# Kernel optimization log

Hardware: AMD Instinct MI355X
Metric: run time of the kernel (lower is better)

The kernel has to match this reference:

```python
import jax, jax.numpy as jnp
import numpy as np

T, B, D = 8192, 8, 512
PRIOR_COUNT = 2
EPS = 1e-5


def setup_inputs() -> dict:
    key = jax.random.key(0)
    ks = jax.random.split(key, 5)
    x = jax.random.normal(ks[0], (T, B, D), dtype=jnp.float32)
    padding_mask = jnp.zeros((B, T), dtype=bool)  # True = padded position
    prior_mean = jax.random.normal(ks[1], (D,), dtype=jnp.float32) * 0.1
    prior_logv = jax.random.normal(ks[2], (D,), dtype=jnp.float32) * 0.1
    weight = jax.random.normal(ks[3], (D,), dtype=jnp.float32) * 0.1
    bias = jax.random.normal(ks[4], (D,), dtype=jnp.float32) * 0.1
    return {"x": x, "prior_mean": prior_mean, "prior_logv": prior_logv,
            "weight": weight, "bias": bias, "padding_mask": padding_mask}


def reference(x, prior_mean, prior_logv, weight, bias, padding_mask):
    # x: (T, B, D); padding_mask: (B, T) with True = pad.
    # Per-timestep Welford running mean/variance (carried across time, skipping
    # padded steps) followed by affine normalization: the TimestepNorm forward.
    gamma = weight + 1.0
    beta = bias
    b = x.shape[1]
    count0 = jnp.full((b,), PRIOR_COUNT, dtype=x.dtype)
    mean0 = jnp.broadcast_to(prior_mean, (b, D)).astype(x.dtype)
    var0 = jnp.broadcast_to(jnp.exp(prior_logv), (b, D)).astype(x.dtype)
    mask_tb = padding_mask.T  # (T, B)

    def step(carry, inp):
        count, mean, var = carry
        xt, mt = inp                                  # xt: (B, D), mt: (B,)
        valid = (~mt).astype(xt.dtype)                # 1 if real token, 0 if pad
        c_new = count + valid
        coef = valid / c_new                          # 0 on padded steps
        delta = xt - mean
        mean_new = mean + coef[:, None] * delta
        # Welford variance update: var += (delta*(x - mean_new) - var)/count
        var_new = var + coef[:, None] * (delta * (xt - mean_new) - var)
        y = (xt - mean_new) * jax.lax.rsqrt(var_new + EPS) * gamma + beta
        return (c_new, mean_new, var_new), y

    (_, _, _), ys = jax.lax.scan(step, (count0, mean0, var0), (x, mask_tb))
    return ys  # (T, B, D), same layout as module output
```

## Files before the change

kernel.cpp:

```cpp
#include <hip/hip_runtime.h>
#include <math.h>


#define T_DIM 8192
#define B_DIM 8
#define D_DIM 512
#define NC    128
#define CT    (T_DIM / NC)
#define BD    (B_DIM * D_DIM)
#define C0    2.0f
#define EPS   1e-5f


__global__ __launch_bounds__(128) void ts_pass1(
    const float* __restrict__ x, const unsigned char* __restrict__ mask,
    float* __restrict__ s1p, float* __restrict__ s2p, float* __restrict__ cnt) {
  const int chunk = blockIdx.x;
  const int b     = blockIdx.y;
  const int tid   = threadIdx.x;
  const int t0    = chunk * CT;
  const float4* xp = (const float4*)x;
  const unsigned char* mrow = mask + b * T_DIM + t0;

  float s1x = 0.f, s1y = 0.f, s1z = 0.f, s1w = 0.f;
  float s2x = 0.f, s2y = 0.f, s2z = 0.f, s2w = 0.f;
  float c = 0.f;
#pragma unroll 4
  for (int i = 0; i < CT; ++i) {
    float valid = mrow[i] ? 0.f : 1.f;
    float4 v = xp[((t0 + i) * B_DIM + b) * (D_DIM / 4) + tid];
    c += valid;
    s1x += valid * v.x; s2x += valid * v.x * v.x;
    s1y += valid * v.y; s2y += valid * v.y * v.y;
    s1z += valid * v.z; s2z += valid * v.z * v.z;
    s1w += valid * v.w; s2w += valid * v.w * v.w;
  }
  const int pidx = chunk * (BD / 4) + b * (D_DIM / 4) + tid;
  ((float4*)s1p)[pidx] = make_float4(s1x, s1y, s1z, s1w);
  ((float4*)s2p)[pidx] = make_float4(s2x, s2y, s2z, s2w);
  if (tid == 0) cnt[chunk * B_DIM + b] = c;
}

__global__ __launch_bounds__(256) void ts_pass2(
    float* __restrict__ s1p, float* __restrict__ s2p, float* __restrict__ cnt) {
  const int gid = blockIdx.x * 256 + threadIdx.x;
  float r1 = 0.f, r2 = 0.f;
#pragma unroll 4
  for (int k = 0; k < NC; ++k) {
    const int idx = k * BD + gid;
    float a1 = s1p[idx], a2 = s2p[idx];
    s1p[idx] = r1; s2p[idx] = r2;
    r1 += a1; r2 += a2;
  }
  if (gid < B_DIM) {
    float rc = 0.f;
    for (int k = 0; k < NC; ++k) {
      float a = cnt[k * B_DIM + gid];
      cnt[k * B_DIM + gid] = rc;
      rc += a;
    }
  }
}

__global__ __launch_bounds__(128) void ts_pass3(
    const float* __restrict__ x, const unsigned char* __restrict__ mask,
    const float* __restrict__ pm, const float* __restrict__ plv,
    const float* __restrict__ w, const float* __restrict__ bias,
    const float* __restrict__ s1p, const float* __restrict__ s2p,
    const float* __restrict__ cnt, float* __restrict__ out) {
  const int chunk = blockIdx.x;
  const int b     = blockIdx.y;
  const int tid   = threadIdx.x;
  const int t0    = chunk * CT;

  float4 pm4 = ((const float4*)pm)[tid];
  float4 lv4 = ((const float4*)plv)[tid];
  float4 g4  = ((const float4*)w)[tid];
  float4 be4 = ((const float4*)bias)[tid];
  g4.x += 1.f; g4.y += 1.f; g4.z += 1.f; g4.w += 1.f;
  float M0x = C0 * pm4.x, M0y = C0 * pm4.y, M0z = C0 * pm4.z, M0w = C0 * pm4.w;
  float V2x = C0 * (__expf(lv4.x) + pm4.x * pm4.x);
  float V2y = C0 * (__expf(lv4.y) + pm4.y * pm4.y);
  float V2z = C0 * (__expf(lv4.z) + pm4.z * pm4.z);
  float V2w = C0 * (__expf(lv4.w) + pm4.w * pm4.w);

  const int pidx = chunk * (BD / 4) + b * (D_DIM / 4) + tid;
  float4 S1 = ((const float4*)s1p)[pidx];
  float4 S2 = ((const float4*)s2p)[pidx];
  float c = C0 + cnt[chunk * B_DIM + b];

  const float4* xp = (const float4*)x;
  float4* op = (float4*)out;
  const unsigned char* mrow = mask + b * T_DIM + t0;

#pragma unroll 4
  for (int i = 0; i < CT; ++i) {
    float valid = mrow[i] ? 0.f : 1.f;
    const int xi = ((t0 + i) * B_DIM + b) * (D_DIM / 4) + tid;
    float4 v = xp[xi];
    c += valid;
    float rc = __builtin_amdgcn_rcpf(c);
    float4 y;
    {
      S1.x += valid * v.x; S2.x += valid * v.x * v.x;
      float M = M0x + S1.x;
      float mean = M * rc;
      float var = (V2x + S2.x - M * M * rc) * rc;
      y.x = (v.x - mean) * __builtin_amdgcn_rsqf(var + EPS) * g4.x + be4.x;
    }
    {
      S1.y += valid * v.y; S2.y += valid * v.y * v.y;
      float M = M0y + S1.y;
      float mean = M * rc;
      float var = (V2y + S2.y - M * M * rc) * rc;
      y.y = (v.y - mean) * __builtin_amdgcn_rsqf(var + EPS) * g4.y + be4.y;
    }
    {
      S1.z += valid * v.z; S2.z += valid * v.z * v.z;
      float M = M0z + S1.z;
      float mean = M * rc;
      float var = (V2z + S2.z - M * M * rc) * rc;
      y.z = (v.z - mean) * __builtin_amdgcn_rsqf(var + EPS) * g4.z + be4.z;
    }
    {
      S1.w += valid * v.w; S2.w += valid * v.w * v.w;
      float M = M0w + S1.w;
      float mean = M * rc;
      float var = (V2w + S2.w - M * M * rc) * rc;
      y.w = (v.w - mean) * __builtin_amdgcn_rsqf(var + EPS) * g4.w + be4.w;
    }
    op[xi] = y;
  }
}

extern "C" void kernel_launch(void* const* d_in, const int* in_sizes, int n_in,
                              void* d_out, int out_size, void* d_ws, size_t ws_size,
                              hipStream_t stream) {
  const float* x    = (const float*)d_in[0];
  const float* pm   = (const float*)d_in[1];
  const float* plv  = (const float*)d_in[2];
  const float* w    = (const float*)d_in[3];
  const float* bias = (const float*)d_in[4];
  const unsigned char* mask = (const unsigned char*)d_in[5];
  float* out = (float*)d_out;

  float* s1p = (float*)d_ws;
  float* s2p = s1p + (size_t)NC * BD;
  float* cnt = s2p + (size_t)NC * BD;

  dim3 grid(NC, B_DIM);
  ts_pass1<<<grid, 128, 0, stream>>>(x, mask, s1p, s2p, cnt);
  ts_pass2<<<BD / 256, 256, 0, stream>>>(s1p, s2p, cnt);
  ts_pass3<<<grid, 128, 0, stream>>>(x, mask, pm, plv, w, bias, s1p, s2p, cnt, out);
}
```

Measured before the change: 299.5 us.

## Fold prefix scan into pass3 and preload mask bytes as 64-bit words

Removes the separate prefix-scan kernel. Each pass3 block now sums the partial sums of all earlier chunks itself before running its output loop. Both the pass1 and pass3 kernels also load the chunk's mask bytes up front as 64-bit words instead of reading a byte per step. This drops one kernel launch and its serial per-column scan over 128 chunks, but later chunks do redundant reads proportional to their chunk index, which adds roughly quadratic partial-sum traffic (mostly cache-resident).

Result: faster. 291.2 us (-2.8%).

```diff
diff --git a/kernel.cpp b/kernel.cpp
--- a/kernel.cpp
+++ b/kernel.cpp
@@ -20,14 +20,19 @@
   const int tid   = threadIdx.x;
   const int t0    = chunk * CT;
   const float4* xp = (const float4*)x;
-  const unsigned char* mrow = mask + b * T_DIM + t0;
+
+  unsigned long long mw[CT / 8];
+  const unsigned long long* m8 =
+      (const unsigned long long*)(mask + b * T_DIM + t0);
+#pragma unroll
+  for (int j = 0; j < CT / 8; ++j) mw[j] = m8[j];
 
   float s1x = 0.f, s1y = 0.f, s1z = 0.f, s1w = 0.f;
   float s2x = 0.f, s2y = 0.f, s2z = 0.f, s2w = 0.f;
   float c = 0.f;
-#pragma unroll 4
+#pragma unroll 8
   for (int i = 0; i < CT; ++i) {
-    float valid = mrow[i] ? 0.f : 1.f;
+    float valid = ((mw[i >> 3] >> ((i & 7) * 8)) & 0xffULL) ? 0.f : 1.f;
     float4 v = xp[((t0 + i) * B_DIM + b) * (D_DIM / 4) + tid];
     c += valid;
     s1x += valid * v.x; s2x += valid * v.x * v.x;
@@ -41,27 +46,6 @@
   if (tid == 0) cnt[chunk * B_DIM + b] = c;
 }
 
-__global__ __launch_bounds__(256) void ts_pass2(
-    float* __restrict__ s1p, float* __restrict__ s2p, float* __restrict__ cnt) {
-  const int gid = blockIdx.x * 256 + threadIdx.x;
-  float r1 = 0.f, r2 = 0.f;
-#pragma unroll 4
-  for (int k = 0; k < NC; ++k) {
-    const int idx = k * BD + gid;
-    float a1 = s1p[idx], a2 = s2p[idx];
-    s1p[idx] = r1; s2p[idx] = r2;
-    r1 += a1; r2 += a2;
-  }
-  if (gid < B_DIM) {
-    float rc = 0.f;
-    for (int k = 0; k < NC; ++k) {
-      float a = cnt[k * B_DIM + gid];
-      cnt[k * B_DIM + gid] = rc;
-      rc += a;
-    }
-  }
-}
-
 __global__ __launch_bounds__(128) void ts_pass3(
     const float* __restrict__ x, const unsigned char* __restrict__ mask,
     const float* __restrict__ pm, const float* __restrict__ plv,
@@ -72,6 +56,24 @@
   const int b     = blockIdx.y;
   const int tid   = threadIdx.x;
   const int t0    = chunk * CT;
+
+  float4 S1 = make_float4(0.f, 0.f, 0.f, 0.f);
+  float4 S2 = make_float4(0.f, 0.f, 0.f, 0.f);
+  float csum = 0.f;
+  {
+    const float4* p1 = (const float4*)s1p;
+    const float4* p2 = (const float4*)s2p;
+    const int col = b * (D_DIM / 4) + tid;
+#pragma unroll 4
+    for (int k = 0; k < chunk; ++k) {
+      float4 a1 = p1[k * (BD / 4) + col];
+      float4 a2 = p2[k * (BD / 4) + col];
+      S1.x += a1.x; S1.y += a1.y; S1.z += a1.z; S1.w += a1.w;
+      S2.x += a2.x; S2.y += a2.y; S2.z += a2.z; S2.w += a2.w;
+      csum += cnt[k * B_DIM + b];
+    }
+  }
+  float c = C0 + csum;
 
   float4 pm4 = ((const float4*)pm)[tid];
   float4 lv4 = ((const float4*)plv)[tid];
@@ -84,18 +86,18 @@
   float V2z = C0 * (__expf(lv4.z) + pm4.z * pm4.z);
   float V2w = C0 * (__expf(lv4.w) + pm4.w * pm4.w);
 
-  const int pidx = chunk * (BD / 4) + b * (D_DIM / 4) + tid;
-  float4 S1 = ((const float4*)s1p)[pidx];
-  float4 S2 = ((const float4*)s2p)[pidx];
-  float c = C0 + cnt[chunk * B_DIM + b];
+  unsigned long long mw[CT / 8];
+  const unsigned long long* m8 =
+      (const unsigned long long*)(mask + b * T_DIM + t0);
+#pragma unroll
+  for (int j = 0; j < CT / 8; ++j) mw[j] = m8[j];
 
   const float4* xp = (const float4*)x;
   float4* op = (float4*)out;
-  const unsigned char* mrow = mask + b * T_DIM + t0;
 
 #pragma unroll 4
   for (int i = 0; i < CT; ++i) {
-    float valid = mrow[i] ? 0.f : 1.f;
+    float valid = ((mw[i >> 3] >> ((i & 7) * 8)) & 0xffULL) ? 0.f : 1.f;
     const int xi = ((t0 + i) * B_DIM + b) * (D_DIM / 4) + tid;
     float4 v = xp[xi];
     c += valid;
@@ -150,6 +152,5 @@
 
   dim3 grid(NC, B_DIM);
   ts_pass1<<<grid, 128, 0, stream>>>(x, mask, s1p, s2p, cnt);
-  ts_pass2<<<BD / 256, 256, 0, stream>>>(s1p, s2p, cnt);
   ts_pass3<<<grid, 128, 0, stream>>>(x, mask, pm, plv, w, bias, s1p, s2p, cnt, out);
 }
```
